# Kernel tuning notes

Measured on AMD Instinct MI355X. Metric: run time of the kernel, lower is better.

## Reference

```python
import jax, jax.numpy as jnp
import numpy as np
import math

B, T, C, H = 2, 2048, 1024, 16
HD = C // H
WINDOW = 256  # local_attn_ctx with attnblocksize=1


def setup_inputs() -> dict:
    key = jax.random.key(0)
    k1, k2, k3 = jax.random.split(key, 3)
    x = jax.random.normal(k1, (B, T, C), dtype=jnp.float32)
    Wqkv = jax.random.normal(k2, (C, 3 * C), dtype=jnp.float32) * 0.02
    bqkv = jnp.zeros((3 * C,), dtype=jnp.float32)
    Wproj = jax.random.normal(k3, (C, C), dtype=jnp.float32) * 0.02
    bproj = jnp.zeros((C,), dtype=jnp.float32)
    # 'local' block-sparse layout at token granularity: causal + sliding window
    i = np.arange(T)[:, None]
    j = np.arange(T)[None, :]
    mask = ((j <= i) & (i - j <= WINDOW)).astype(np.int32)
    return {"x": x, "Wqkv": Wqkv, "bqkv": bqkv, "Wproj": Wproj, "bproj": bproj,
            "mask": jnp.asarray(mask)}


def reference(x, Wqkv, bqkv, Wproj, bproj, mask):
    Bb, Tt, Cc = x.shape
    qkv = (x @ Wqkv + bqkv).reshape(Bb, Tt, 3, H, HD)  # [B,T,3,H,hd]
    q = jnp.transpose(qkv[:, :, 0], (0, 2, 1, 3))  # [B,H,T,hd]
    k = jnp.transpose(qkv[:, :, 1], (0, 2, 1, 3))
    v = jnp.transpose(qkv[:, :, 2], (0, 2, 1, 3))
    scale = 1.0 / math.sqrt(HD)
    att = jnp.einsum('bhqd,bhkd->bhqk', q, k) * scale  # dense T x T scores
    att = jnp.where(mask[:Tt, :Tt] == 0, -jnp.inf, att)
    att = jax.nn.softmax(att, axis=-1)
    y = jnp.einsum('bhqk,bhkd->bhqd', att, v)
    y = jnp.transpose(y, (0, 2, 1, 3)).reshape(Bb, Tt, Cc)
    return y @ Wproj + bproj
```

## Files before the change

### kernel.cpp

```cpp
#include <hip/hip_runtime.h>
#include <hip/hip_bf16.h>
#include <math.h>

typedef __bf16 bf16;
typedef __attribute__((ext_vector_type(8))) __bf16 bf16x8;
typedef __attribute__((ext_vector_type(4))) __bf16 bf16x4;
typedef __attribute__((ext_vector_type(4))) float f32x4;

#define B_  2
#define T_  2048
#define C_  1024
#define H_  16
#define HD_ 64
#define WIN_ 256

#define GLOAD16(g, l)                                                        \
  __builtin_amdgcn_global_load_lds(                                          \
      (const __attribute__((address_space(1))) void*)(g),                    \
      (__attribute__((address_space(3))) void*)(l), 16, 0, 0)

__device__ inline void bar() {
  asm volatile("" ::: "memory");
  __builtin_amdgcn_s_barrier();
  asm volatile("" ::: "memory");
}


__global__ __launch_bounds__(256) void prologue_k(const float* __restrict__ x,
                                                  bf16* __restrict__ xb,
                                                  const float* __restrict__ Wqkv,
                                                  bf16* __restrict__ wqkvT,
                                                  const float* __restrict__ Wproj,
                                                  bf16* __restrict__ wprojT) {
  __shared__ float t[32][33];
  const int blk = blockIdx.x;
  const int tid = threadIdx.x;

  if (blk < 4096) {
    const int idx = blk * 256 + tid;
    const float4 v = ((const float4*)x)[idx];
    bf16x4 o;
    o[0] = (bf16)v.x; o[1] = (bf16)v.y; o[2] = (bf16)v.z; o[3] = (bf16)v.w;
    ((bf16x4*)xb)[idx] = o;
    return;
  }

  const float* W; bf16* WT; int N, tb;
  if (blk < 4096 + 3072) { tb = blk - 4096; W = Wqkv;  WT = wqkvT;  N = 3 * C_; }
  else                   { tb = blk - 7168; W = Wproj; WT = wprojT; N = C_;     }
  const int xt = N / 32;
  const int n0 = (tb % xt) * 32, k0 = (tb / xt) * 32;
  const int tx = tid & 31, ty = tid >> 5;

  #pragma unroll
  for (int i = 0; i < 32; i += 8)
    t[ty + i][tx] = W[(size_t)(k0 + ty + i) * N + (n0 + tx)];
  __syncthreads();
  #pragma unroll
  for (int i = 0; i < 32; i += 8)
    WT[(size_t)(n0 + ty + i) * C_ + (k0 + tx)] = (bf16)t[tx][ty + i];
}


template <int TM, int TN, int WM, int WN, int MINW, int MODE>
__global__ __launch_bounds__(WM * WN * 64, MINW)
void gemm_db_k(const bf16* __restrict__ A, const bf16* __restrict__ Bt,
               const float* __restrict__ bias,
               void* __restrict__ out0, void* __restrict__ out1,
               int M, int N, int K) {
  constexpr int NW    = WM * WN;
  constexpr int WROWS = TM / WM;
  constexpr int WCOLS = TN / WN;
  constexpr int FM    = WROWS / 16;
  constexpr int FN    = WCOLS / 16;
  constexpr int NCH   = (TM + TN) / 8;
  constexpr int CPW   = NCH / NW;

  const int bm = blockIdx.x * TM;
  const int bn = blockIdx.y * TN;
  const int tid  = threadIdx.x;
  const int wid  = tid >> 6;
  const int lane = tid & 63;
  const int wr = wid / WN;
  const int wc = wid % WN;
  const int lr = lane & 15;
  const int g  = lane >> 4;

  __shared__ bf16 As[2][TM * 64];
  __shared__ bf16 Bs[2][TN * 64];

  f32x4 acc[FM][FN] = {};

  const int sr = lane >> 3;
  const int sc = ((lane & 7) ^ sr) << 3;

  #define STG(p_, u_)                                                        \
    do {                                                                     \
      _Pragma("unroll")                                                      \
      for (int i = 0; i < CPW; ++i) {                                        \
        const int c = wid * CPW + i;                                         \
        if (c < TM / 8) {                                                    \
          GLOAD16(A + (size_t)(bm + c * 8 + sr) * K + (u_) * 64 + sc,        \
                  &As[p_][c * 8 * 64]);                                      \
        } else {                                                             \
          GLOAD16(Bt + (size_t)(bn + (c - TM / 8) * 8 + sr) * K + (u_) * 64 + sc, \
                  &Bs[p_][(c - TM / 8) * 8 * 64]);                           \
        }                                                                    \
      }                                                                      \
    } while (0)

  const int NT = K >> 6;
  const int kc0 = ((0 + g) ^ (lr & 7)) << 3;
  const int kc1 = ((4 + g) ^ (lr & 7)) << 3;

  STG(0, 0);
  asm volatile("s_waitcnt vmcnt(0)" ::: "memory");
  __builtin_amdgcn_s_barrier();
  asm volatile("" ::: "memory");

  for (int u = 0; u < NT; ++u) {
    const int p = u & 1;
    if (u + 1 < NT) {
      STG(p ^ 1, u + 1);
      asm volatile("s_waitcnt vmcnt(%0)" :: "i"(CPW) : "memory");
    } else {
      asm volatile("s_waitcnt vmcnt(0)" ::: "memory");
    }
    bar();

    const bf16* Ar = &As[p][(wr * WROWS + lr) * 64];
    const bf16* Br = &Bs[p][(wc * WCOLS + lr) * 64];
    #pragma unroll
    for (int s = 0; s < 2; ++s) {
      const int kc = s ? kc1 : kc0;
      bf16x8 av[FM], bvv[FN];
      #pragma unroll
      for (int m = 0; m < FM; ++m)
        av[m] = *(const bf16x8*)(Ar + m * 16 * 64 + kc);
      #pragma unroll
      for (int n = 0; n < FN; ++n)
        bvv[n] = *(const bf16x8*)(Br + n * 16 * 64 + kc);
      __builtin_amdgcn_s_setprio(1);
      #pragma unroll
      for (int m = 0; m < FM; ++m)
        #pragma unroll
        for (int n = 0; n < FN; ++n)
          acc[m][n] = __builtin_amdgcn_mfma_f32_16x16x32_bf16(av[m], bvv[n], acc[m][n], 0, 0, 0);
      __builtin_amdgcn_s_setprio(0);
    }
    bar();
  }
  #undef STG

  const int orow = g * 4;
  #pragma unroll
  for (int n = 0; n < FN; ++n) {
    const int nbase = bn + wc * WCOLS + n * 16;
    const int gn = nbase + lr;
    const float bv_ = bias[gn];
    #pragma unroll
    for (int m = 0; m < FM; ++m) {
      const int gm0 = bm + wr * WROWS + m * 16 + orow;
      if (MODE == 0) {
        #pragma unroll
        for (int r = 0; r < 4; ++r)
          ((float*)out0)[(size_t)(gm0 + r) * N + gn] = acc[m][n][r] + bv_;
      } else {
        if (nbase < 2 * C_) {
          #pragma unroll
          for (int r = 0; r < 4; ++r)
            ((bf16*)out0)[(size_t)(gm0 + r) * (2 * C_) + gn] = (bf16)(acc[m][n][r] + bv_);
        } else {
          const int vcol = gn - 2 * C_;
          const int h = vcol >> 6, d = vcol & 63;
          const int b = gm0 >> 11, tok = gm0 & (T_ - 1);
          bf16x4 o;
          #pragma unroll
          for (int r = 0; r < 4; ++r) o[r] = (bf16)(acc[m][n][r] + bv_);
          *(bf16x4*)&((bf16*)out1)[(((size_t)b * H_ + h) * HD_ + d) * T_ + tok] = o;
        }
      }
    }
  }
}


__global__ __launch_bounds__(256) void attn_mfma_k(const bf16* __restrict__ qk,
                                                   const bf16* __restrict__ vt,
                                                   bf16* __restrict__ y) {
  const int q0 = blockIdx.x * 64;
  const int h  = blockIdx.y;
  const int b  = blockIdx.z;
  const int tid  = threadIdx.x;
  const int wid  = tid >> 6;
  const int lane = tid & 63;
  const int lr = lane & 15;
  const int g  = lane >> 4;

  __shared__ bf16 Ks[64][72];
  __shared__ bf16 Vs[64][72];
  __shared__ bf16 Ps[4][16][72];

  const int qrow = q0 + wid * 16 + lr;
  const bf16* qptr = qk + ((size_t)(b * T_ + qrow)) * (2 * C_) + h * HD_;
  bf16x8 qf[2];
  qf[0] = *(const bf16x8*)(qptr + g * 8);
  qf[1] = *(const bf16x8*)(qptr + 32 + g * 8);

  float m = -1e30f, l = 0.f;
  f32x4 yacc[4] = {};

  const int kt_lo = (blockIdx.x >= 4) ? (int)blockIdx.x - 4 : 0;
  for (int kt = kt_lo; kt <= (int)blockIdx.x; ++kt) {
    __syncthreads();
    #pragma unroll
    for (int i = 0; i < 2; ++i) {
      int cc = tid + i * 256;
      int rr = cc >> 3;
      int c0 = (cc & 7) * 8;
      *(bf16x8*)&Ks[rr][c0] = *(const bf16x8*)&qk[((size_t)(b * T_) + kt * 64 + rr) * (2 * C_) + C_ + h * HD_ + c0];
      *(bf16x8*)&Vs[rr][c0] = *(const bf16x8*)&vt[(((size_t)b * H_ + h) * HD_ + rr) * T_ + kt * 64 + c0];
    }
    __syncthreads();

    f32x4 sacc[4] = {};
    #pragma unroll
    for (int t = 0; t < 4; ++t)
      #pragma unroll
      for (int s = 0; s < 2; ++s)
        sacc[t] = __builtin_amdgcn_mfma_f32_16x16x32_bf16(
            *(const bf16x8*)&Ks[t * 16 + lr][s * 32 + g * 8], qf[s], sacc[t], 0, 0, 0);

    float pv[4][4];
    float rmax = -1e30f;
    #pragma unroll
    for (int t = 0; t < 4; ++t)
      #pragma unroll
      for (int r = 0; r < 4; ++r) {
        const int key = kt * 64 + t * 16 + g * 4 + r;
        const bool valid = (key <= qrow) && (qrow - key <= WIN_);
        const float sv = valid ? sacc[t][r] * 0.125f : -__builtin_inff();
        pv[t][r] = sv;
        rmax = fmaxf(rmax, sv);
      }
    rmax = fmaxf(rmax, __shfl_xor(rmax, 16));
    rmax = fmaxf(rmax, __shfl_xor(rmax, 32));

    const float mnew = fmaxf(m, rmax);
    const float alpha = __expf(m - mnew);
    m = mnew;
    float lsum = 0.f;
    #pragma unroll
    for (int t = 0; t < 4; ++t)
      #pragma unroll
      for (int r = 0; r < 4; ++r) {
        const float e = __expf(pv[t][r] - mnew);
        pv[t][r] = e;
        lsum += e;
      }
    lsum += __shfl_xor(lsum, 16);
    lsum += __shfl_xor(lsum, 32);
    l = l * alpha + lsum;

    #pragma unroll
    for (int t = 0; t < 4; ++t) {
      bf16x4 pk;
      #pragma unroll
      for (int r = 0; r < 4; ++r) pk[r] = (bf16)pv[t][r];
      *(bf16x4*)&Ps[wid][lr][t * 16 + g * 4] = pk;
    }

    float al[4];
    #pragma unroll
    for (int r = 0; r < 4; ++r) al[r] = __shfl(alpha, g * 4 + r);
    #pragma unroll
    for (int t = 0; t < 4; ++t)
      #pragma unroll
      for (int r = 0; r < 4; ++r) yacc[t][r] *= al[r];

    bf16x8 pf[2];
    pf[0] = *(const bf16x8*)&Ps[wid][lr][g * 8];
    pf[1] = *(const bf16x8*)&Ps[wid][lr][32 + g * 8];
    #pragma unroll
    for (int t = 0; t < 4; ++t)
      #pragma unroll
      for (int s = 0; s < 2; ++s)
        yacc[t] = __builtin_amdgcn_mfma_f32_16x16x32_bf16(
            pf[s], *(const bf16x8*)&Vs[t * 16 + lr][s * 32 + g * 8], yacc[t], 0, 0, 0);
  }

  float li[4];
  #pragma unroll
  for (int r = 0; r < 4; ++r) li[r] = 1.f / __shfl(l, g * 4 + r);
  #pragma unroll
  for (int t = 0; t < 4; ++t)
    #pragma unroll
    for (int r = 0; r < 4; ++r) {
      const int tok = q0 + wid * 16 + g * 4 + r;
      y[((size_t)(b * T_ + tok)) * C_ + h * HD_ + t * 16 + lr] = (bf16)(yacc[t][r] * li[r]);
    }
}


extern "C" void kernel_launch(void* const* d_in, const int* in_sizes, int n_in,
                              void* d_out, int out_size, void* d_ws, size_t ws_size,
                              hipStream_t stream) {
  const float* x     = (const float*)d_in[0];
  const float* Wqkv  = (const float*)d_in[1];
  const float* bqkv  = (const float*)d_in[2];
  const float* Wproj = (const float*)d_in[3];
  const float* bproj = (const float*)d_in[4];
  float* out = (float*)d_out;

  const size_t SZ_QK  = (size_t)B_ * T_ * 2 * C_ * sizeof(bf16);
  const size_t SZ_VT  = (size_t)B_ * H_ * HD_ * T_ * sizeof(bf16);
  const size_t SZ_XB  = (size_t)B_ * T_ * C_ * sizeof(bf16);
  const size_t SZ_WQT = (size_t)3 * C_ * C_ * sizeof(bf16);
  const size_t SZ_WPT = (size_t)C_ * C_ * sizeof(bf16);
  const size_t NEED   = SZ_QK + SZ_VT + SZ_XB + SZ_WQT + SZ_WPT + SZ_XB;
  if (ws_size < NEED) return;

  char* ws = (char*)d_ws;
  bf16* qkb    = (bf16*)(ws);
  bf16* vtb    = (bf16*)(ws + SZ_QK);
  bf16* xb     = (bf16*)(ws + SZ_QK + SZ_VT);
  bf16* wqkvT  = (bf16*)(ws + SZ_QK + SZ_VT + SZ_XB);
  bf16* wprojT = (bf16*)(ws + SZ_QK + SZ_VT + SZ_XB + SZ_WQT);
  bf16* yb     = (bf16*)(ws + SZ_QK + SZ_VT + SZ_XB + SZ_WQT + SZ_WPT);

  prologue_k<<<8192, 256, 0, stream>>>(x, xb, Wqkv, wqkvT, Wproj, wprojT);

  gemm_db_k<128, 192, 2, 4, 4, 2><<<dim3((B_ * T_) / 128, (3 * C_) / 192), 512, 0, stream>>>(
      xb, wqkvT, bqkv, qkb, vtb, B_ * T_, 3 * C_, C_);

  attn_mfma_k<<<dim3(T_ / 64, H_, B_), 256, 0, stream>>>(qkb, vtb, yb);

  gemm_db_k<64, 128, 2, 2, 2, 0><<<dim3((B_ * T_) / 64, C_ / 128), 256, 0, stream>>>(
      yb, wprojT, bproj, out, nullptr, B_ * T_, C_, C_);
}
```

Baseline: 81.24 us.

## Load K/V tiles into LDS via direct global-to-LDS with XOR swizzle

The attention kernel now fills the K and V tiles with global_load_lds 16-byte direct copies instead of register round-trips, laid out unpadded with an XOR swizzle so MFMA operand reads stay bank-conflict free. The barrier placement moves to a wait-then-barrier at load and a trailing barrier after the PV MFMAs, and s_setprio raises wave priority around the MFMA blocks. This cuts VGPR staging and LDS store instructions, at the risk of exposing the full load latency since nothing is double-buffered.

New measurement: 81.53 us. About the same (+0.4%).

```diff
diff --git a/kernel.cpp b/kernel.cpp
--- a/kernel.cpp
+++ b/kernel.cpp
@@ -197,8 +197,8 @@
   const int lr = lane & 15;
   const int g  = lane >> 4;
 
-  __shared__ bf16 Ks[64][72];
-  __shared__ bf16 Vs[64][72];
+  __shared__ bf16 Ks[64 * 64];
+  __shared__ bf16 Vs[64 * 64];
   __shared__ bf16 Ps[4][16][72];
 
   const int qrow = q0 + wid * 16 + lr;
@@ -210,26 +210,34 @@
   float m = -1e30f, l = 0.f;
   f32x4 yacc[4] = {};
 
+  const int sr = lane >> 3;
+  const int sc = ((lane & 7) ^ sr) << 3;
+  const int kc0 = ((0 + g) ^ (lr & 7)) << 3;
+  const int kc1 = ((4 + g) ^ (lr & 7)) << 3;
+
   const int kt_lo = (blockIdx.x >= 4) ? (int)blockIdx.x - 4 : 0;
   for (int kt = kt_lo; kt <= (int)blockIdx.x; ++kt) {
-    __syncthreads();
     #pragma unroll
     for (int i = 0; i < 2; ++i) {
-      int cc = tid + i * 256;
-      int rr = cc >> 3;
-      int c0 = (cc & 7) * 8;
-      *(bf16x8*)&Ks[rr][c0] = *(const bf16x8*)&qk[((size_t)(b * T_) + kt * 64 + rr) * (2 * C_) + C_ + h * HD_ + c0];
-      *(bf16x8*)&Vs[rr][c0] = *(const bf16x8*)&vt[(((size_t)b * H_ + h) * HD_ + rr) * T_ + kt * 64 + c0];
-    }
-    __syncthreads();
+      const int c = wid * 2 + i;
+      GLOAD16(qk + ((size_t)(b * T_) + kt * 64 + c * 8 + sr) * (2 * C_) + C_ + h * HD_ + sc,
+              &Ks[c * 8 * 64]);
+      GLOAD16(vt + (((size_t)b * H_ + h) * HD_ + c * 8 + sr) * T_ + kt * 64 + sc,
+              &Vs[c * 8 * 64]);
+    }
+    asm volatile("s_waitcnt vmcnt(0)" ::: "memory");
+    bar();
 
     f32x4 sacc[4] = {};
-    #pragma unroll
-    for (int t = 0; t < 4; ++t)
-      #pragma unroll
-      for (int s = 0; s < 2; ++s)
-        sacc[t] = __builtin_amdgcn_mfma_f32_16x16x32_bf16(
-            *(const bf16x8*)&Ks[t * 16 + lr][s * 32 + g * 8], qf[s], sacc[t], 0, 0, 0);
+    __builtin_amdgcn_s_setprio(1);
+    #pragma unroll
+    for (int t = 0; t < 4; ++t) {
+      sacc[t] = __builtin_amdgcn_mfma_f32_16x16x32_bf16(
+          *(const bf16x8*)&Ks[(t * 16 + lr) * 64 + kc0], qf[0], sacc[t], 0, 0, 0);
+      sacc[t] = __builtin_amdgcn_mfma_f32_16x16x32_bf16(
+          *(const bf16x8*)&Ks[(t * 16 + lr) * 64 + kc1], qf[1], sacc[t], 0, 0, 0);
+    }
+    __builtin_amdgcn_s_setprio(0);
 
     float pv[4][4];
     float rmax = -1e30f;
@@ -281,12 +289,16 @@
     bf16x8 pf[2];
     pf[0] = *(const bf16x8*)&Ps[wid][lr][g * 8];
     pf[1] = *(const bf16x8*)&Ps[wid][lr][32 + g * 8];
-    #pragma unroll
-    for (int t = 0; t < 4; ++t)
-      #pragma unroll
-      for (int s = 0; s < 2; ++s)
-        yacc[t] = __builtin_amdgcn_mfma_f32_16x16x32_bf16(
-            pf[s], *(const bf16x8*)&Vs[t * 16 + lr][s * 32 + g * 8], yacc[t], 0, 0, 0);
+    __builtin_amdgcn_s_setprio(1);
+    #pragma unroll
+    for (int t = 0; t < 4; ++t) {
+      yacc[t] = __builtin_amdgcn_mfma_f32_16x16x32_bf16(
+          pf[0], *(const bf16x8*)&Vs[(t * 16 + lr) * 64 + kc0], yacc[t], 0, 0, 0);
+      yacc[t] = __builtin_amdgcn_mfma_f32_16x16x32_bf16(
+          pf[1], *(const bf16x8*)&Vs[(t * 16 + lr) * 64 + kc1], yacc[t], 0, 0, 0);
+    }
+    __builtin_amdgcn_s_setprio(0);
+    bar();
   }
 
   float li[4];
```
